# Optimization experiments

Hardware: AMD Instinct MI355X
Metric: run time of the kernel (lower is better)

The kernel has to match this reference:

```python
import jax, jax.numpy as jnp
import numpy as np

B, F, CTX, HID, L, NB = 16384, 64, 128, 512, 8, 2


def setup_inputs() -> dict:
    key = jax.random.key(0)
    ks = jax.random.split(key, 8)
    inputs = jax.random.normal(ks[0], (B, F), jnp.float32)
    context = jax.random.normal(ks[1], (B, CTX), jnp.float32)
    n_id = F // 2                      # identity features per coupling layer
    in_dim = n_id + CTX                # coupling net input = identity half + context
    out_dim = F                        # 2 * num_transform_features (shift | scale)
    s_in = 1.0 / np.sqrt(in_dim)
    s_h = 1.0 / np.sqrt(HID)
    W_in = jax.random.uniform(ks[2], (L, in_dim, HID), jnp.float32, -s_in, s_in)
    b_in = jax.random.uniform(ks[3], (L, HID), jnp.float32, -s_in, s_in)
    W_h = jax.random.uniform(ks[4], (L, NB, HID, HID), jnp.float32, -s_h, s_h)
    b_h = jax.random.uniform(ks[5], (L, NB, HID), jnp.float32, -s_h, s_h)
    # output layer init: normal(0, 0.01) weight, zero bias (as in torch source)
    W_out = 0.01 * jax.random.normal(ks[6], (L, HID, out_dim), jnp.float32)
    b_out = jnp.zeros((L, out_dim), jnp.float32)
    # fixed random permutations between coupling layers (nflows RandomPermutation buffers)
    rng = np.random.RandomState(42)
    perms = jnp.asarray(np.stack([rng.permutation(F) for _ in range(L - 1)]), jnp.int32)
    return dict(inputs=inputs, context=context, W_in=W_in, b_in=b_in,
                W_h=W_h, b_h=b_h, W_out=W_out, b_out=b_out, perms=perms)


def reference(inputs, context, W_in, b_in, W_h, b_h, W_out, b_out, perms):
    F_ = inputs.shape[-1]
    n_layers = W_in.shape[0]
    n_blocks = W_h.shape[1]
    nt = F_ // 2  # num transform features
    even_idx = jnp.arange(0, F_, 2)
    odd_idx = jnp.arange(1, F_, 2)
    x = jnp.clip(inputs, -1.0, 1.0)
    logdet = jnp.zeros(x.shape[0], x.dtype)
    for i in range(n_layers):
        # mask[::2]=1 for even layers -> mask>0 (even indices) are TRANSFORM features
        if i % 2 == 0:
            t_idx, id_idx = even_idx, odd_idx
        else:
            t_idx, id_idx = odd_idx, even_idx
        id_split = x[:, id_idx]   # [B, nt]
        tr_split = x[:, t_idx]    # [B, nt]
        h = jax.nn.relu(jnp.concatenate([id_split, context], -1) @ W_in[i] + b_in[i])
        for j in range(n_blocks):
            h = jax.nn.relu(h @ W_h[i, j] + b_h[i, j])
        p = h @ W_out[i] + b_out[i]            # [B, 2*nt]
        shift = p[:, :nt]
        scale = jax.nn.sigmoid(p[:, nt:] + 2.0) + 1e-3
        logdet = logdet + jnp.sum(jnp.log(scale), axis=-1)
        x = x.at[:, t_idx].set(tr_split * scale + shift).at[:, id_idx].set(id_split)
        if i < n_layers - 1:
            x = x[:, perms[i]]
    return jnp.clip(x, -1.0, 1.0), logdet
```

## Files before the change

kernel.cpp:

```cpp
#include <hip/hip_runtime.h>


typedef float v4f  __attribute__((ext_vector_type(4)));
typedef float v16f __attribute__((ext_vector_type(16)));
typedef int   v4i  __attribute__((ext_vector_type(4)));
typedef int   v8i  __attribute__((ext_vector_type(8)));
typedef unsigned char uchar;
typedef unsigned long long ull;

#define BATCH 16384
#define NF    64
#define NCTX  128
#define NL    8

#define RS     528
#define HHALF  256
#define AST    208
#define AHALF  96

#define WSCALE     16.0f
#define WSCALE_INV 0.0625f

#define WIN_EPL   (192 * 512)
#define WH_EPB    (512 * 512)
#define WOUT_EPL  (512 * 64)
#define OFF_WIN   ((size_t)0)
#define OFF_WH    ((size_t)(8 * WIN_EPL))
#define OFF_WOUT  (OFF_WH + (size_t)(16 * WH_EPB))
#define TOT_PACK_ELEMS (OFF_WOUT + (size_t)(8 * WOUT_EPL))
#define NEED_WS   (TOT_PACK_ELEMS)

#define NU_IN   192
#define NU_H    1024
#define NU_OUT  128
#define NU_TOT  (NU_IN + NU_H + NU_OUT)

template<bool HI>
__device__ __forceinline__ unsigned int pk2(float a, float b, unsigned int old) {
    return __builtin_amdgcn_cvt_pk_fp8_f32(a, b, old, HI);
}
__device__ __forceinline__ uchar q8(float v) {
    return (uchar)(__builtin_amdgcn_cvt_pk_fp8_f32(v, v, 0u, false) & 0xffu);
}

__global__ __launch_bounds__(256) void pack_weights_kernel(
    const float* __restrict__ W_in,
    const float* __restrict__ W_h,
    const float* __restrict__ W_out,
    unsigned char* __restrict__ ws) {
    const int wid  = (blockIdx.x * blockDim.x + threadIdx.x) >> 6;
    const int lane = threadIdx.x & 63;
    if (wid >= NU_TOT) return;

    if (wid < NU_IN + NU_H) {
        const float* src;
        uchar* dstbase;
        int kb, khalf, g, rawK;
        if (wid < NU_IN) {
            int i = wid / 24, r = wid % 24;
            kb = r >> 3; khalf = (r >> 2) & 1; g = r & 3;
            src = W_in + (size_t)i * (160 * 512); rawK = 160;
            dstbase = ws + OFF_WIN + (size_t)i * WIN_EPL + kb * 32768;
        } else {
            int u = wid - NU_IN;
            int ij = u >> 6, r = u & 63;
            kb = r >> 3; khalf = (r >> 2) & 1; g = r & 3;
            src = W_h + (size_t)ij * WH_EPB; rawK = 512;
            dstbase = ws + OFF_WH + (size_t)ij * WH_EPB + kb * 32768;
        }
        const int pig = (g == 1) ? 2 : (g == 2) ? 1 : g;
        const int k0  = kb * 64 + khalf * 32 + pig * 8;
        const int n0  = lane * 8;
        float v[8][8];
        if (k0 < rawK) {
#pragma unroll
            for (int j = 0; j < 8; ++j) {
                const float* p = src + (size_t)(k0 + j) * 512 + n0;
                float4 a = ((const float4*)p)[0];
                float4 b = ((const float4*)p)[1];
                v[j][0] = a.x * WSCALE; v[j][1] = a.y * WSCALE;
                v[j][2] = a.z * WSCALE; v[j][3] = a.w * WSCALE;
                v[j][4] = b.x * WSCALE; v[j][5] = b.y * WSCALE;
                v[j][6] = b.z * WSCALE; v[j][7] = b.w * WSCALE;
            }
        } else {
#pragma unroll
            for (int j = 0; j < 8; ++j)
#pragma unroll
                for (int nn = 0; nn < 8; ++nn) v[j][nn] = 0.f;
        }
        uchar* dst = dstbase +
            ((lane >> 2) * 64 + 32 * khalf + (lane & 3) * 8) * 32 + g * 8;
#pragma unroll
        for (int nn = 0; nn < 8; ++nn) {
            uint2 o;
            o.x = pk2<false>(v[0][nn], v[1][nn], 0u);
            o.x = pk2<true >(v[2][nn], v[3][nn], o.x);
            o.y = pk2<false>(v[4][nn], v[5][nn], 0u);
            o.y = pk2<true >(v[6][nn], v[7][nn], o.y);
            *(uint2*)(dst + nn * 32) = o;
        }
    } else {
        int u = wid - (NU_IN + NU_H);
        int i = u >> 4, kc = u & 15;
        const float* src = W_out + (size_t)i * WOUT_EPL;
        float v[32];
#pragma unroll
        for (int k = 0; k < 32; ++k)
            v[k] = src[(size_t)(kc * 32 + k) * 64 + lane] * WSCALE;
        uchar* dst = ws + OFF_WOUT + (size_t)i * 32768 +
                     (size_t)(kc * 4 + (lane >> 4)) * 512;
#pragma unroll
        for (int ks = 0; ks < 4; ++ks) {
            uint2 o;
            o.x = pk2<false>(v[ks * 8 + 0], v[ks * 8 + 1], 0u);
            o.x = pk2<true >(v[ks * 8 + 2], v[ks * 8 + 3], o.x);
            o.y = pk2<false>(v[ks * 8 + 4], v[ks * 8 + 5], 0u);
            o.y = pk2<true >(v[ks * 8 + 6], v[ks * 8 + 7], o.y);
            *(uint2*)(dst + (ks * 16 + (lane & 15)) * 8) = o;
        }
    }
}

__device__ __forceinline__ v16f mfma32(ull a, ull b, v16f c) {
    return __builtin_amdgcn_mfma_f32_32x32x16_fp8_fp8((long)a, (long)b, c, 0, 0, 0);
}
__device__ __forceinline__ v4f mfma16(ull a, ull b, v4f c) {
    return __builtin_amdgcn_mfma_f32_16x16x32_fp8_fp8((long)a, (long)b, c, 0, 0, 0);
}
__device__ __forceinline__ v16f mfma64(v8i a, v8i b, v16f c) {
    return __builtin_amdgcn_mfma_scale_f32_32x32x64_f8f6f4(
        a, b, c, 0, 0, 0, 0x7f7f7f7f, 0, 0x7f7f7f7f);
}

template<int NKB>
__device__ __forceinline__ void gemm32mx(
    const uchar* __restrict__ wpk,
    const float* __restrict__ bias,
    const uchar* __restrict__ Abuf, int ast, int halfoff,
    uchar* __restrict__ Obuf,
    int pair, int lane)
{
    const int l31 = lane & 31, hl = lane >> 5;
    v16f a00, a01, a10, a11;
#pragma unroll
    for (int r = 0; r < 16; ++r) { a00[r] = 0.f; a01[r] = 0.f;
                                   a10[r] = 0.f; a11[r] = 0.f; }
    const uchar* aLo0 = Abuf + l31 * ast + hl * 16;
    const uchar* aHi0 = aLo0 + halfoff;
    const uchar* aLo1 = aLo0 + 32 * ast;
    const uchar* aHi1 = aHi0 + 32 * ast;
    const uchar* bp = wpk + (size_t)(pair * 128 + lane) * 32;

    auto loadB = [&](int s, int kb) -> v8i {
        if (kb >= NKB) kb = NKB - 1;
        const uchar* p = bp + s * 2048 + (size_t)kb * 32768;
        v4i lo = *(const v4i*)p;
        v4i hi = *(const v4i*)(p + 16);
        return __builtin_shufflevector(lo, hi, 0, 1, 2, 3, 4, 5, 6, 7);
    };
    auto loadA = [&](const uchar* lo_, const uchar* hi_, int kb) -> v8i {
        if (kb >= NKB) kb = NKB - 1;
        v4i lo = *(const v4i*)(lo_ + kb * 32);
        v4i hi = *(const v4i*)(hi_ + kb * 32);
        return __builtin_shufflevector(lo, hi, 0, 1, 2, 3, 4, 5, 6, 7);
    };

    v8i xA0 = loadA(aLo0, aHi0, 0), xA1 = loadA(aLo1, aHi1, 0);
    v8i xB0 = loadA(aLo0, aHi0, 1), xB1 = loadA(aLo1, aHi1, 1);
    v8i b00 = loadB(0, 0), b10 = loadB(1, 0);
    v8i b01 = loadB(0, 1), b11 = loadB(1, 1);
#pragma unroll 1
    for (int kb = 0; kb + 1 < NKB; kb += 2) {
        a00 = mfma64(b00, xA0, a00);
        a01 = mfma64(b00, xA1, a01);
        a10 = mfma64(b10, xA0, a10);
        a11 = mfma64(b10, xA1, a11);
        xA0 = loadA(aLo0, aHi0, kb + 2);
        xA1 = loadA(aLo1, aHi1, kb + 2);
        b00 = loadB(0, kb + 2);
        b10 = loadB(1, kb + 2);
        a00 = mfma64(b01, xB0, a00);
        a01 = mfma64(b01, xB1, a01);
        a10 = mfma64(b11, xB0, a10);
        a11 = mfma64(b11, xB1, a11);
        xB0 = loadA(aLo0, aHi0, kb + 3);
        xB1 = loadA(aLo1, aHi1, kb + 3);
        b01 = loadB(0, kb + 3);
        b11 = loadB(1, kb + 3);
    }
    if constexpr (NKB & 1) {
        a00 = mfma64(b00, xA0, a00);
        a01 = mfma64(b00, xA1, a01);
        a10 = mfma64(b10, xA0, a10);
        a11 = mfma64(b10, xA1, a11);
    }

    const uchar* ob0 = Obuf + l31 * RS + 4 * hl;
    const uchar* ob1 = ob0 + 32 * RS;
    auto emit = [&](const v16f& am0, const v16f& am1, int strip) {
#pragma unroll
        for (int q = 0; q < 4; ++q) {
            const int n0 = strip * 32 + q * 8 + 4 * hl;
            float4 bv = *(const float4*)(bias + n0);
            unsigned int u0, u1;
            u0 = pk2<false>(fmaxf(fmaf(am0[4 * q + 0], WSCALE_INV, bv.x), 0.f),
                            fmaxf(fmaf(am0[4 * q + 1], WSCALE_INV, bv.y), 0.f), 0u);
            u0 = pk2<true >(fmaxf(fmaf(am0[4 * q + 2], WSCALE_INV, bv.z), 0.f),
                            fmaxf(fmaf(am0[4 * q + 3], WSCALE_INV, bv.w), 0.f), u0);
            u1 = pk2<false>(fmaxf(fmaf(am1[4 * q + 0], WSCALE_INV, bv.x), 0.f),
                            fmaxf(fmaf(am1[4 * q + 1], WSCALE_INV, bv.y), 0.f), 0u);
            u1 = pk2<true >(fmaxf(fmaf(am1[4 * q + 2], WSCALE_INV, bv.z), 0.f),
                            fmaxf(fmaf(am1[4 * q + 3], WSCALE_INV, bv.w), 0.f), u1);
            const int g = strip * 4 + q;
            const int off = (g & 1) * HHALF + ((g >> 1) << 3);
            *(unsigned int*)(ob0 + off) = u0;
            *(unsigned int*)(ob1 + off) = u1;
        }
    };
    emit(a00, a01, pair * 2 + 0);
    emit(a10, a11, pair * 2 + 1);
}

template<int KC>
__device__ __forceinline__ void gemm32_raw(
    const float* __restrict__ wraw,
    const float* __restrict__ bias,
    const uchar* __restrict__ Abuf, int ast, int ahalf,
    uchar* __restrict__ Obuf,
    int strip, int lane)
{
    constexpr int P = KC / 2;
    const int l31 = lane & 31, hl = lane >> 5;
    v16f acc0, acc1;
#pragma unroll
    for (int r = 0; r < 16; ++r) { acc0[r] = 0.f; acc1[r] = 0.f; }
    const uchar* a0p = Abuf + l31 * ast + hl * ahalf;
    const uchar* a1p = a0p + 32 * ast;

    auto loadB = [&](int kc) -> ull {
        if (kc >= KC) kc = KC - 1;
        int n  = strip * 32 + l31;
        int k0 = kc * 16 + hl * 8;
        unsigned int lo, hi;
        lo = pk2<false>(wraw[(size_t)(k0 + 0) * 512 + n] * WSCALE,
                        wraw[(size_t)(k0 + 1) * 512 + n] * WSCALE, 0u);
        lo = pk2<true >(wraw[(size_t)(k0 + 2) * 512 + n] * WSCALE,
                        wraw[(size_t)(k0 + 3) * 512 + n] * WSCALE, lo);
        hi = pk2<false>(wraw[(size_t)(k0 + 4) * 512 + n] * WSCALE,
                        wraw[(size_t)(k0 + 5) * 512 + n] * WSCALE, 0u);
        hi = pk2<true >(wraw[(size_t)(k0 + 6) * 512 + n] * WSCALE,
                        wraw[(size_t)(k0 + 7) * 512 + n] * WSCALE, hi);
        return ((ull)hi << 32) | (ull)lo;
    };

    ull b0 = loadB(0), b1 = loadB(1), b2 = loadB(2), b3 = loadB(3);
    int p2 = 0;
#pragma unroll 1
    for (; p2 + 1 < P; p2 += 2) {
        ulonglong2 Aa0 = *(const ulonglong2*)(a0p + p2 * 16);
        ulonglong2 Aa1 = *(const ulonglong2*)(a1p + p2 * 16);
        acc0 = mfma32(Aa0.x, b0, acc0);
        acc1 = mfma32(Aa1.x, b0, acc1);
        b0 = loadB(2 * p2 + 4);
        acc0 = mfma32(Aa0.y, b1, acc0);
        acc1 = mfma32(Aa1.y, b1, acc1);
        b1 = loadB(2 * p2 + 5);
        ulonglong2 Ab0 = *(const ulonglong2*)(a0p + p2 * 16 + 16);
        ulonglong2 Ab1 = *(const ulonglong2*)(a1p + p2 * 16 + 16);
        acc0 = mfma32(Ab0.x, b2, acc0);
        acc1 = mfma32(Ab1.x, b2, acc1);
        b2 = loadB(2 * p2 + 6);
        acc0 = mfma32(Ab0.y, b3, acc0);
        acc1 = mfma32(Ab1.y, b3, acc1);
        b3 = loadB(2 * p2 + 7);
    }
    if constexpr (P & 1) {
        ulonglong2 Aa0 = *(const ulonglong2*)(a0p + (P - 1) * 16);
        ulonglong2 Aa1 = *(const ulonglong2*)(a1p + (P - 1) * 16);
        acc0 = mfma32(Aa0.x, b0, acc0);
        acc1 = mfma32(Aa1.x, b0, acc1);
        acc0 = mfma32(Aa0.y, b1, acc0);
        acc1 = mfma32(Aa1.y, b1, acc1);
    }

    const int n = strip * 32 + l31;
    const int nb = ((n >> 3) & 1) * HHALF + ((n >> 4) << 3) + (n & 7);
    const float bv = bias[n];
#pragma unroll
    for (int reg = 0; reg < 16; ++reg) {
        int row = (reg & 3) + 8 * (reg >> 2) + 4 * hl;
        float v0 = fmaxf(fmaf(acc0[reg], WSCALE_INV, bv), 0.f);
        Obuf[row * RS + nb] = q8(v0);
        float v1 = fmaxf(fmaf(acc1[reg], WSCALE_INV, bv), 0.f);
        Obuf[(row + 32) * RS + nb] = q8(v1);
    }
}

template<bool PACKED>
__device__ __forceinline__ float gemm16_fused(
    const uchar* __restrict__ wpk,
    const float* __restrict__ wraw,
    const float* __restrict__ bias,
    const uchar* __restrict__ Abuf,
    float* __restrict__ xbuf,
    const int* __restrict__ ct,
    int par, int w, int lane)
{
    const int quad = lane >> 4, l15 = lane & 15;
    const int mtb  = w >> 1;
    const int npair = w & 1;
    const int ntb0 = npair, ntb1 = npair + 2;
    const int row  = mtb * 16 + l15;
    v4f acc0, acc1;
    acc0[0] = acc0[1] = acc0[2] = acc0[3] = 0.f;
    acc1[0] = acc1[1] = acc1[2] = acc1[3] = 0.f;
    const uchar* ap = Abuf + row * RS + (quad & 1) * HHALF + ((quad >> 1) << 3);
    const uchar* bp0 =
        PACKED ? wpk + (size_t)(ntb0 * 64 + lane) * 8 : (const uchar*)0;
    const uchar* bp1 =
        PACKED ? wpk + (size_t)(ntb1 * 64 + lane) * 8 : (const uchar*)0;
    constexpr int KC = 16;

    auto loadB = [&](const uchar* bp, int ntb, int kc) -> ull {
        if (kc >= KC) kc = KC - 1;
        if constexpr (PACKED) {
            return *(const ull*)(bp + (size_t)kc * 2048);
        } else {
            int n  = ntb * 16 + l15;
            int k0 = kc * 32 + quad * 8;
            unsigned int lo, hi;
            lo = pk2<false>(wraw[(size_t)(k0 + 0) * 64 + n] * WSCALE,
                            wraw[(size_t)(k0 + 1) * 64 + n] * WSCALE, 0u);
            lo = pk2<true >(wraw[(size_t)(k0 + 2) * 64 + n] * WSCALE,
                            wraw[(size_t)(k0 + 3) * 64 + n] * WSCALE, lo);
            hi = pk2<false>(wraw[(size_t)(k0 + 4) * 64 + n] * WSCALE,
                            wraw[(size_t)(k0 + 5) * 64 + n] * WSCALE, 0u);
            hi = pk2<true >(wraw[(size_t)(k0 + 6) * 64 + n] * WSCALE,
                            wraw[(size_t)(k0 + 7) * 64 + n] * WSCALE, hi);
            return ((ull)hi << 32) | (ull)lo;
        }
    };
    auto rdA = [&](int kc) -> ull {
        if (kc >= KC) kc = KC - 1;
        return *(const ull*)(ap + kc * 16);
    };

    ull a0 = rdA(0), a1 = rdA(1), a2 = rdA(2), a3 = rdA(3);
    ull u0 = loadB(bp0, ntb0, 0), u1 = loadB(bp0, ntb0, 1);
    ull u2 = loadB(bp0, ntb0, 2), u3 = loadB(bp0, ntb0, 3);
    ull v0 = loadB(bp1, ntb1, 0), v1 = loadB(bp1, ntb1, 1);
    ull v2 = loadB(bp1, ntb1, 2), v3 = loadB(bp1, ntb1, 3);
    int kc = 0;
#pragma unroll 1
    for (; kc + 3 < KC; kc += 4) {
        acc0 = mfma16(u0, a0, acc0); acc1 = mfma16(v0, a0, acc1);
        a0 = rdA(kc + 4);
        u0 = loadB(bp0, ntb0, kc + 4); v0 = loadB(bp1, ntb1, kc + 4);
        acc0 = mfma16(u1, a1, acc0); acc1 = mfma16(v1, a1, acc1);
        a1 = rdA(kc + 5);
        u1 = loadB(bp0, ntb0, kc + 5); v1 = loadB(bp1, ntb1, kc + 5);
        acc0 = mfma16(u2, a2, acc0); acc1 = mfma16(v2, a2, acc1);
        a2 = rdA(kc + 6);
        u2 = loadB(bp0, ntb0, kc + 6); v2 = loadB(bp1, ntb1, kc + 6);
        acc0 = mfma16(u3, a3, acc0); acc1 = mfma16(v3, a3, acc1);
        a3 = rdA(kc + 7);
        u3 = loadB(bp0, ntb0, kc + 7); v3 = loadB(bp1, ntb1, kc + 7);
    }

    const int n0 = ntb0 * 16 + quad * 4;
    float ld = 0.f;
#pragma unroll
    for (int r = 0; r < 4; ++r) {
        float shiftv = fmaf(acc0[r], WSCALE_INV, bias[n0 + r]);
        float z      = fmaf(acc1[r], WSCALE_INV, bias[32 + n0 + r]) + 2.0f;
        float s      = 1.0f / (1.0f + __expf(-z)) + 0.001f;
        int sc = n0 + r;
        int tc = ct[2 * sc + par];
        float xo = xbuf[row * NF + tc];
        xbuf[row * NF + tc] = xo * s + shiftv;
        ld += __logf(s);
    }
    return ld;
}

template<bool PACKED>
__global__ __launch_bounds__(512, 2) void flow_kernel(
    const float* __restrict__ inputs,
    const float* __restrict__ ctx,
    const float* __restrict__ W_in,  const float* __restrict__ b_in,
    const float* __restrict__ W_h,   const float* __restrict__ b_h,
    const float* __restrict__ W_out, const float* __restrict__ b_out,
    const int*   __restrict__ perms,
    const uchar* __restrict__ wpk,
    float* __restrict__ out)
{
    __shared__ __align__(16) uchar hbuf0[64 * RS];
    __shared__ __align__(16) uchar hbuf1[64 * RS];
    __shared__ __align__(16) uchar abuf[64 * AST];
    __shared__ __align__(16) float xbuf[64 * NF];
    __shared__ int Ctab[NL * NF];

    const int tid  = threadIdx.x;
    const int wave = tid >> 6;
    const int lane = tid & 63;
    const int trow = tid >> 3;
    const int t8   = tid & 7;
    const int row0 = blockIdx.x * 64;

    {
        int i = tid >> 6, c = tid & 63;
        int idx = c;
        for (int k = i - 1; k >= 0; --k) idx = perms[k * NF + idx];
        Ctab[tid] = idx;
    }
    {
#pragma unroll
        for (int j = 0; j < 2; ++j) {
            float4 v = ((const float4*)(inputs + (size_t)row0 * NF))[tid + j * 512];
            v.x = fminf(fmaxf(v.x, -1.f), 1.f);
            v.y = fminf(fmaxf(v.y, -1.f), 1.f);
            v.z = fminf(fmaxf(v.z, -1.f), 1.f);
            v.w = fminf(fmaxf(v.w, -1.f), 1.f);
            ((float4*)xbuf)[tid + j * 512] = v;
        }
    }
    {
        const float* crow = ctx + (size_t)(row0 + trow) * NCTX + t8 * 16;
        float4 f0 = ((const float4*)crow)[0];
        float4 f1 = ((const float4*)crow)[1];
        float4 f2 = ((const float4*)crow)[2];
        float4 f3 = ((const float4*)crow)[3];
        uint2 ck0, ck1;
        ck0.x = pk2<false>(f0.x, f0.y, 0u);
        ck0.x = pk2<true >(f0.z, f0.w, ck0.x);
        ck0.y = pk2<false>(f1.x, f1.y, 0u);
        ck0.y = pk2<true >(f1.z, f1.w, ck0.y);
        ck1.x = pk2<false>(f2.x, f2.y, 0u);
        ck1.x = pk2<true >(f2.z, f2.w, ck1.x);
        ck1.y = pk2<false>(f3.x, f3.y, 0u);
        ck1.y = pk2<true >(f3.z, f3.w, ck1.y);
        *(uint2*)(abuf + trow * AST + (2 + t8) * 8) = ck0;
        *(uint2*)(abuf + trow * AST + AHALF + (2 + t8) * 8) = ck1;
    }
    if (tid < 256) {
        int r = tid >> 2, q = tid & 3;
        *(ull*)(abuf + r * AST + (q & 1) * AHALF + 80 + ((q >> 1) << 3)) = 0ULL;
    }
    float ld_acc = 0.f;
    __syncthreads();

#pragma unroll 1
    for (int i = 0; i < NL; ++i) {
        const int par = i & 1;
        const int idp = par ^ 1;
        const int* ct = Ctab + i * NF;

        if (t8 < 4) {
            const float* xr = xbuf + trow * NF;
            uint2 idv;
            idv.x = pk2<false>(xr[ct[2 * (t8 * 8 + 0) + idp]],
                               xr[ct[2 * (t8 * 8 + 1) + idp]], 0u);
            idv.x = pk2<true >(xr[ct[2 * (t8 * 8 + 2) + idp]],
                               xr[ct[2 * (t8 * 8 + 3) + idp]], idv.x);
            idv.y = pk2<false>(xr[ct[2 * (t8 * 8 + 4) + idp]],
                               xr[ct[2 * (t8 * 8 + 5) + idp]], 0u);
            idv.y = pk2<true >(xr[ct[2 * (t8 * 8 + 6) + idp]],
                               xr[ct[2 * (t8 * 8 + 7) + idp]], idv.y);
            *(uint2*)(abuf + trow * AST + (t8 & 1) * AHALF + ((t8 >> 1) << 3)) = idv;
        }
        __syncthreads();

        if constexpr (PACKED) {
            gemm32mx<3>(wpk + OFF_WIN + (size_t)i * WIN_EPL, b_in + i * 512,
                        abuf, AST, AHALF, hbuf0, wave, lane);
            __syncthreads();
            gemm32mx<8>(wpk + OFF_WH + (size_t)(i * 2 + 0) * WH_EPB,
                        b_h + (i * 2 + 0) * 512,
                        hbuf0, RS, HHALF, hbuf1, wave, lane);
            __syncthreads();
            gemm32mx<8>(wpk + OFF_WH + (size_t)(i * 2 + 1) * WH_EPB,
                        b_h + (i * 2 + 1) * 512,
                        hbuf1, RS, HHALF, hbuf0, wave, lane);
            __syncthreads();
        } else {
            gemm32_raw<10>(W_in + (size_t)i * (160 * 512), b_in + i * 512,
                           abuf, AST, AHALF, hbuf0, wave * 2 + 0, lane);
            gemm32_raw<10>(W_in + (size_t)i * (160 * 512), b_in + i * 512,
                           abuf, AST, AHALF, hbuf0, wave * 2 + 1, lane);
            __syncthreads();
            gemm32_raw<32>(W_h + (size_t)(i * 2 + 0) * WH_EPB,
                           b_h + (i * 2 + 0) * 512,
                           hbuf0, RS, HHALF, hbuf1, wave * 2 + 0, lane);
            gemm32_raw<32>(W_h + (size_t)(i * 2 + 0) * WH_EPB,
                           b_h + (i * 2 + 0) * 512,
                           hbuf0, RS, HHALF, hbuf1, wave * 2 + 1, lane);
            __syncthreads();
            gemm32_raw<32>(W_h + (size_t)(i * 2 + 1) * WH_EPB,
                           b_h + (i * 2 + 1) * 512,
                           hbuf1, RS, HHALF, hbuf0, wave * 2 + 0, lane);
            gemm32_raw<32>(W_h + (size_t)(i * 2 + 1) * WH_EPB,
                           b_h + (i * 2 + 1) * 512,
                           hbuf1, RS, HHALF, hbuf0, wave * 2 + 1, lane);
            __syncthreads();
        }
        ld_acc += gemm16_fused<PACKED>(
            PACKED ? wpk + OFF_WOUT + (size_t)i * WOUT_EPL : (const uchar*)0,
            W_out + (size_t)i * WOUT_EPL, b_out + i * 64,
            hbuf0, xbuf, ct, par, wave, lane);
        __syncthreads();
    }

    {
        const int* c7 = Ctab + 7 * NF;
#pragma unroll
        for (int j = 0; j < 2; ++j) {
            int p = tid + j * 512;
            int r = p >> 4, c0 = (p & 15) * 4;
            const float* xr = xbuf + r * NF;
            float4 v;
            v.x = fminf(fmaxf(xr[c7[c0 + 0]], -1.f), 1.f);
            v.y = fminf(fmaxf(xr[c7[c0 + 1]], -1.f), 1.f);
            v.z = fminf(fmaxf(xr[c7[c0 + 2]], -1.f), 1.f);
            v.w = fminf(fmaxf(xr[c7[c0 + 3]], -1.f), 1.f);
            ((float4*)(out + (size_t)row0 * NF))[p] = v;
        }
    }
    {
        float* lbuf = (float*)abuf;
        const int rrow = (wave >> 1) * 16 + (lane & 15);
        const int slot = (wave & 1) * 4 + (lane >> 4);
        lbuf[rrow * 8 + slot] = ld_acc;
        __syncthreads();
        if (tid < 64) {
            float s = 0.f;
#pragma unroll
            for (int k = 0; k < 8; ++k) s += lbuf[tid * 8 + k];
            out[(size_t)BATCH * NF + row0 + tid] = s;
        }
    }
}

extern "C" void kernel_launch(void* const* d_in, const int* in_sizes, int n_in,
                              void* d_out, int out_size, void* d_ws, size_t ws_size,
                              hipStream_t stream) {
    const float* inputs  = (const float*)d_in[0];
    const float* context = (const float*)d_in[1];
    const float* W_in    = (const float*)d_in[2];
    const float* b_in    = (const float*)d_in[3];
    const float* W_h     = (const float*)d_in[4];
    const float* b_h     = (const float*)d_in[5];
    const float* W_out   = (const float*)d_in[6];
    const float* b_out   = (const float*)d_in[7];
    const int*   perms   = (const int*)d_in[8];
    float* out = (float*)d_out;

    if (ws_size >= (size_t)NEED_WS) {
        uchar* ws = (uchar*)d_ws;
        const int total_threads = NU_TOT * 64;
        pack_weights_kernel<<<(total_threads + 255) / 256, 256, 0, stream>>>(
            W_in, W_h, W_out, ws);
        flow_kernel<true><<<256, 512, 0, stream>>>(
            inputs, context, W_in, b_in, W_h, b_h, W_out, b_out, perms, ws, out);
    } else {
        flow_kernel<false><<<256, 512, 0, stream>>>(
            inputs, context, W_in, b_in, W_h, b_h, W_out, b_out, perms,
            (const uchar*)0, out);
    }
}
```

Measured before the change: 200.1 us.

## Prefetch next GEMM weights before barriers and use LDS-only barriers

Issues the first weight (B operand) global loads for each upcoming GEMM stage before the barrier separating stages, so their latency overlaps the barrier wait and the tail of the previous stage. Replaces __syncthreads with a barrier that waits only on LDS counters (lgkmcnt), so in-flight global prefetches are not drained at each barrier. This raises register pressure from the held prefetch values. It also relies on the prefetched global loads being waited on correctly before use.

```diff
diff --git a/kernel.cpp b/kernel.cpp
--- a/kernel.cpp
+++ b/kernel.cpp
@@ -41,6 +41,12 @@
 }
 __device__ __forceinline__ uchar q8(float v) {
     return (uchar)(__builtin_amdgcn_cvt_pk_fp8_f32(v, v, 0u, false) & 0xffu);
+}
+
+__device__ __forceinline__ void bar_lds() {
+    asm volatile("s_waitcnt lgkmcnt(0)" ::: "memory");
+    __builtin_amdgcn_s_barrier();
+    asm volatile("" ::: "memory");
 }
 
 __global__ __launch_bounds__(256) void pack_weights_kernel(
@@ -133,13 +139,45 @@
         a, b, c, 0, 0, 0, 0x7f7f7f7f, 0, 0x7f7f7f7f);
 }
 
+__device__ __forceinline__ v8i ldv8(const uchar* p) {
+    v4i lo = *(const v4i*)p;
+    v4i hi = *(const v4i*)(p + 16);
+    return __builtin_shufflevector(lo, hi, 0, 1, 2, 3, 4, 5, 6, 7);
+}
+
+struct BPre  { v8i b00, b10, b01, b11; };
+struct BPre16 { ull u0, u1, u2, u3, v0, v1, v2, v3; } ;
+
+__device__ __forceinline__ BPre prefB(const uchar* __restrict__ wpk,
+                                      int pair, int lane) {
+    const uchar* bp = wpk + (size_t)(pair * 128 + lane) * 32;
+    BPre r;
+    r.b00 = ldv8(bp);
+    r.b10 = ldv8(bp + 2048);
+    r.b01 = ldv8(bp + 32768);
+    r.b11 = ldv8(bp + 32768 + 2048);
+    return r;
+}
+__device__ __forceinline__ BPre16 prefB16(const uchar* __restrict__ wpk,
+                                          int w, int lane) {
+    const int npair = w & 1;
+    const uchar* bp0 = wpk + (size_t)(npair * 64 + lane) * 8;
+    const uchar* bp1 = wpk + (size_t)((npair + 2) * 64 + lane) * 8;
+    BPre16 r;
+    r.u0 = *(const ull*)(bp0);        r.u1 = *(const ull*)(bp0 + 2048);
+    r.u2 = *(const ull*)(bp0 + 4096); r.u3 = *(const ull*)(bp0 + 6144);
+    r.v0 = *(const ull*)(bp1);        r.v1 = *(const ull*)(bp1 + 2048);
+    r.v2 = *(const ull*)(bp1 + 4096); r.v3 = *(const ull*)(bp1 + 6144);
+    return r;
+}
+
 template<int NKB>
 __device__ __forceinline__ void gemm32mx(
     const uchar* __restrict__ wpk,
     const float* __restrict__ bias,
     const uchar* __restrict__ Abuf, int ast, int halfoff,
     uchar* __restrict__ Obuf,
-    int pair, int lane)
+    int pair, int lane, BPre pre)
 {
     const int l31 = lane & 31, hl = lane >> 5;
     v16f a00, a01, a10, a11;
@@ -154,10 +192,7 @@
 
     auto loadB = [&](int s, int kb) -> v8i {
         if (kb >= NKB) kb = NKB - 1;
-        const uchar* p = bp + s * 2048 + (size_t)kb * 32768;
-        v4i lo = *(const v4i*)p;
-        v4i hi = *(const v4i*)(p + 16);
-        return __builtin_shufflevector(lo, hi, 0, 1, 2, 3, 4, 5, 6, 7);
+        return ldv8(bp + s * 2048 + (size_t)kb * 32768);
     };
     auto loadA = [&](const uchar* lo_, const uchar* hi_, int kb) -> v8i {
         if (kb >= NKB) kb = NKB - 1;
@@ -168,8 +203,8 @@
 
     v8i xA0 = loadA(aLo0, aHi0, 0), xA1 = loadA(aLo1, aHi1, 0);
     v8i xB0 = loadA(aLo0, aHi0, 1), xB1 = loadA(aLo1, aHi1, 1);
-    v8i b00 = loadB(0, 0), b10 = loadB(1, 0);
-    v8i b01 = loadB(0, 1), b11 = loadB(1, 1);
+    v8i b00 = pre.b00, b10 = pre.b10;
+    v8i b01 = pre.b01, b11 = pre.b11;
 #pragma unroll 1
     for (int kb = 0; kb + 1 < NKB; kb += 2) {
         a00 = mfma64(b00, xA0, a00);
@@ -305,7 +340,7 @@
     const uchar* __restrict__ Abuf,
     float* __restrict__ xbuf,
     const int* __restrict__ ct,
-    int par, int w, int lane)
+    int par, int w, int lane, BPre16 pre)
 {
     const int quad = lane >> 4, l15 = lane & 15;
     const int mtb  = w >> 1;
@@ -347,10 +382,16 @@
     };
 
     ull a0 = rdA(0), a1 = rdA(1), a2 = rdA(2), a3 = rdA(3);
-    ull u0 = loadB(bp0, ntb0, 0), u1 = loadB(bp0, ntb0, 1);
-    ull u2 = loadB(bp0, ntb0, 2), u3 = loadB(bp0, ntb0, 3);
-    ull v0 = loadB(bp1, ntb1, 0), v1 = loadB(bp1, ntb1, 1);
-    ull v2 = loadB(bp1, ntb1, 2), v3 = loadB(bp1, ntb1, 3);
+    ull u0, u1, u2, u3, v0, v1, v2, v3;
+    if constexpr (PACKED) {
+        u0 = pre.u0; u1 = pre.u1; u2 = pre.u2; u3 = pre.u3;
+        v0 = pre.v0; v1 = pre.v1; v2 = pre.v2; v3 = pre.v3;
+    } else {
+        u0 = loadB(bp0, ntb0, 0); u1 = loadB(bp0, ntb0, 1);
+        u2 = loadB(bp0, ntb0, 2); u3 = loadB(bp0, ntb0, 3);
+        v0 = loadB(bp1, ntb1, 0); v1 = loadB(bp1, ntb1, 1);
+        v2 = loadB(bp1, ntb1, 2); v3 = loadB(bp1, ntb1, 3);
+    }
     int kc = 0;
 #pragma unroll 1
     for (; kc + 3 < KC; kc += 4) {
@@ -448,7 +489,10 @@
         *(ull*)(abuf + r * AST + (q & 1) * AHALF + 80 + ((q >> 1) << 3)) = 0ULL;
     }
     float ld_acc = 0.f;
-    __syncthreads();
+
+    BPre preN;
+    if constexpr (PACKED) preN = prefB(wpk + OFF_WIN, wave, lane);
+    bar_lds();
 
 #pragma unroll 1
     for (int i = 0; i < NL; ++i) {
@@ -469,46 +513,56 @@
                                xr[ct[2 * (t8 * 8 + 7) + idp]], idv.y);
             *(uint2*)(abuf + trow * AST + (t8 & 1) * AHALF + ((t8 >> 1) << 3)) = idv;
         }
-        __syncthreads();
+        bar_lds();
 
         if constexpr (PACKED) {
+            const uchar* wg1 = wpk + OFF_WH + (size_t)(i * 2 + 0) * WH_EPB;
+            const uchar* wg2 = wpk + OFF_WH + (size_t)(i * 2 + 1) * WH_EPB;
+            const uchar* wg3 = wpk + OFF_WOUT + (size_t)i * WOUT_EPL;
             gemm32mx<3>(wpk + OFF_WIN + (size_t)i * WIN_EPL, b_in + i * 512,
-                        abuf, AST, AHALF, hbuf0, wave, lane);
-            __syncthreads();
-            gemm32mx<8>(wpk + OFF_WH + (size_t)(i * 2 + 0) * WH_EPB,
-                        b_h + (i * 2 + 0) * 512,
-                        hbuf0, RS, HHALF, hbuf1, wave, lane);
-            __syncthreads();
-            gemm32mx<8>(wpk + OFF_WH + (size_t)(i * 2 + 1) * WH_EPB,
-                        b_h + (i * 2 + 1) * 512,
-                        hbuf1, RS, HHALF, hbuf0, wave, lane);
-            __syncthreads();
+                        abuf, AST, AHALF, hbuf0, wave, lane, preN);
+            BPre pre1 = prefB(wg1, wave, lane);
+            bar_lds();
+            gemm32mx<8>(wg1, b_h + (i * 2 + 0) * 512,
+                        hbuf0, RS, HHALF, hbuf1, wave, lane, pre1);
+            BPre pre2 = prefB(wg2, wave, lane);
+            bar_lds();
+            gemm32mx<8>(wg2, b_h + (i * 2 + 1) * 512,
+                        hbuf1, RS, HHALF, hbuf0, wave, lane, pre2);
+            BPre16 pre3 = prefB16(wg3, wave, lane);
+            bar_lds();
+            ld_acc += gemm16_fused<true>(
+                wg3, W_out + (size_t)i * WOUT_EPL, b_out + i * 64,
+                hbuf0, xbuf, ct, par, wave, lane, pre3);
+            preN = prefB(wpk + OFF_WIN + (size_t)((i + 1) & 7) * WIN_EPL,
+                         wave, lane);
+            bar_lds();
         } else {
             gemm32_raw<10>(W_in + (size_t)i * (160 * 512), b_in + i * 512,
                            abuf, AST, AHALF, hbuf0, wave * 2 + 0, lane);
             gemm32_raw<10>(W_in + (size_t)i * (160 * 512), b_in + i * 512,
                            abuf, AST, AHALF, hbuf0, wave * 2 + 1, lane);
-            __syncthreads();
+            bar_lds();
             gemm32_raw<32>(W_h + (size_t)(i * 2 + 0) * WH_EPB,
                            b_h + (i * 2 + 0) * 512,
                            hbuf0, RS, HHALF, hbuf1, wave * 2 + 0, lane);
             gemm32_raw<32>(W_h + (size_t)(i * 2 + 0) * WH_EPB,
                            b_h + (i * 2 + 0) * 512,
                            hbuf0, RS, HHALF, hbuf1, wave * 2 + 1, lane);
-            __syncthreads();
+            bar_lds();
             gemm32_raw<32>(W_h + (size_t)(i * 2 + 1) * WH_EPB,
                            b_h + (i * 2 + 1) * 512,
                            hbuf1, RS, HHALF, hbuf0, wave * 2 + 0, lane);
             gemm32_raw<32>(W_h + (size_t)(i * 2 + 1) * WH_EPB,
                            b_h + (i * 2 + 1) * 512,
                            hbuf1, RS, HHALF, hbuf0, wave * 2 + 1, lane);
-            __syncthreads();
-        }
-        ld_acc += gemm16_fused<PACKED>(
-            PACKED ? wpk + OFF_WOUT + (size_t)i * WOUT_EPL : (const uchar*)0,
-            W_out + (size_t)i * WOUT_EPL, b_out + i * 64,
-            hbuf0, xbuf, ct, par, wave, lane);
-        __syncthreads();
+            bar_lds();
+            BPre16 dummy{};
+            ld_acc += gemm16_fused<false>(
+                (const uchar*)0, W_out + (size_t)i * WOUT_EPL, b_out + i * 64,
+                hbuf0, xbuf, ct, par, wave, lane, dummy);
+            bar_lds();
+        }
     }
 
     {
@@ -531,7 +585,7 @@
         const int rrow = (wave >> 1) * 16 + (lane & 15);
         const int slot = (wave & 1) * 4 + (lane >> 4);
         lbuf[rrow * 8 + slot] = ld_acc;
-        __syncthreads();
+        bar_lds();
         if (tid < 64) {
             float s = 0.f;
 #pragma unroll
```

Result: faster. 194.5 us (-2.8%).
